# Optimization experiments

Measured on AMD Instinct MI355X. Metric: run time of the kernel, lower is better.

## Reference

```python
import jax, jax.numpy as jnp
import numpy as np

STATE_DIM = 32
OBS_DIM = 16
PROCESS_VAR = 1e-4
MEAS_VAR = 1e-2
B = 2048
T = 64


def setup_inputs() -> dict:
    key = jax.random.key(0)
    k1, k2, k3 = jax.random.split(key, 3)
    state0 = jax.random.normal(k1, (B, STATE_DIM), dtype=jnp.float32)
    # Initial covariance P = I (per torch __init__), broadcast over batch
    cov0 = jnp.broadcast_to(jnp.eye(STATE_DIM, dtype=jnp.float32), (B, STATE_DIM, STATE_DIM))
    measurements = jax.random.normal(k2, (B, T, OBS_DIM), dtype=jnp.float32)
    # Parameters per torch __init__: F = eye, H = randn, Q = pv*I, R = mv*I
    F = jnp.eye(STATE_DIM, dtype=jnp.float32)
    H = jax.random.normal(k3, (OBS_DIM, STATE_DIM), dtype=jnp.float32)
    Q = PROCESS_VAR * jnp.eye(STATE_DIM, dtype=jnp.float32)
    R = MEAS_VAR * jnp.eye(OBS_DIM, dtype=jnp.float32)
    return {"state0": state0, "cov0": cov0, "measurements": measurements,
            "F": F, "H": H, "Q": Q, "R": R}


def reference(state0, cov0, measurements, F, H, Q, R):
    """Run Kalman predict+update over T timesteps; return filtered states (B,T,S)."""

    def step(carry, z):
        x, P = carry  # x: (B,S), P: (B,S,S); z: (B,O)
        # --- predict ---
        x_pred = x @ F.T                                   # F @ x per batch
        P_pred = jnp.einsum('ij,bjk,lk->bil', F, P, F) + Q  # F P F^T + Q
        # --- update ---
        y = x_pred @ H.T                                   # predicted measurement (B,O)
        innov = z - y
        S = jnp.einsum('ij,bjk,lk->bil', H, P_pred, H) + R  # (B,O,O)
        S_inv = jnp.linalg.inv(S)
        K = jnp.einsum('bij,kj,bkl->bil', P_pred, H, S_inv)  # P H^T S^{-1}, (B,S,O)
        x_new = x_pred + jnp.einsum('bij,bj->bi', K, innov)
        P_new = P_pred - jnp.einsum('bij,jk,bkl->bil', K, H, P_pred)  # (I - K H) P
        return (x_new, P_new), x_new

    # scan over time axis: measurements (B,T,O) -> (T,B,O)
    (_, _), states = jax.lax.scan(step, (state0, cov0), jnp.swapaxes(measurements, 0, 1))
    return jnp.swapaxes(states, 0, 1)  # (B,T,S)
```

## Files before the change

kernel.cpp:

```cpp
#include <hip/hip_runtime.h>
#include <math.h>


#define S_DIM 32
#define O_DIM 16
#define HS 36
#define CW 8
#define NTHR 576

__device__ __forceinline__ float rdlanef(float v, int srcLane) {
    return __uint_as_float(
        (unsigned int)__builtin_amdgcn_readlane((int)__float_as_uint(v), srcLane));
}

__global__ __launch_bounds__(NTHR) void kf_fused(
    const float* __restrict__ state0,
    const float* __restrict__ cov0,
    const float* __restrict__ meas,
    const float* __restrict__ Fm,
    const float* __restrict__ Hm,
    const float* __restrict__ Qm,
    const float* __restrict__ Rm,
    float* __restrict__ out,
    int T, int B)
{
    const int tid = threadIdx.x;

    __shared__ float P  [S_DIM*33];
    __shared__ float Fs [S_DIM*33];
    __shared__ float Qs [S_DIM*33];
    __shared__ float Tp [S_DIM*33];
    __shared__ float Hs [O_DIM*HS];
    __shared__ float HQ [O_DIM*HS];
    __shared__ float HPs[O_DIM*HS];
    __shared__ float KT [2][O_DIM*33];
    __shared__ float Sg [O_DIM*17];
    __shared__ float Rs [O_DIM*17];
    __shared__ float S0g[O_DIM*17];
    __shared__ float xs [CW][32];
    __shared__ float iv [CW][16];
    __shared__ int notId, notDiag, notScal, convFlag, convT;
    __shared__ float cupad[13000];

    if (tid == 0) {
        ((volatile float*)cupad)[0] = 0.f;
        notId = 0; notDiag = 0; notScal = 0; convFlag = 0; convT = 0;
    }

    for (int i = tid; i < S_DIM*S_DIM; i += NTHR) {
        int r = i >> 5, c = i & 31;
        P [r*33+c] = cov0[i];
        Fs[r*33+c] = Fm[i];
        Qs[r*33+c] = Qm[i];
    }
    for (int i = tid; i < O_DIM*S_DIM; i += NTHR) {
        int r = i >> 5, c = i & 31;
        Hs[r*HS+c] = Hm[i];
    }
    for (int i = tid; i < O_DIM*O_DIM; i += NTHR) {
        int r = i >> 4, c = i & 15;
        Rs[r*17+c] = Rm[i];
    }
    __syncthreads();

    {
        bool badI = false, badD = false, badS = false;
        float r00 = Rs[0];
        for (int i = tid; i < S_DIM*S_DIM; i += NTHR) {
            int r = i >> 5, c = i & 31;
            if (Fs[r*33+c] != ((r == c) ? 1.0f : 0.0f)) badI = true;
        }
        for (int i = tid; i < O_DIM*O_DIM; i += NTHR) {
            int r = i >> 4, c = i & 15;
            if (r != c && Rs[r*17+c] != 0.0f) badD = true;
            if (r == c && Rs[r*17+c] != r00)  badS = true;
        }
        if (badI) notId = 1;
        if (badD) notDiag = 1;
        if (badS) notScal = 1;
    }
    __syncthreads();
    const bool fId   = (notId == 0);
    const bool rDiag = (notDiag == 0);
    const bool rScal = rDiag && (notScal == 0);

    const int wv = tid >> 6;
    const int l  = tid & 63;
    const int s  = l & 31;
    const int h  = l >> 5;
    const int o  = l & 15;
    const int q  = l >> 4;
    const int wi = (wv >= 1) ? (wv - 1) : 0;
    const bool isCons = (wv >= 1);
    long bb = (long)blockIdx.x * CW + wi;
    const long b = (bb < B) ? bb : (B - 1);

    float4 h0v, h1v;
    {
        const float4* Hv = (const float4*)(Hm + o*S_DIM + q*8);
        h0v = Hv[0]; h1v = Hv[1];
    }

    float x = 0.f;
    if (isCons) {
        x = state0[b*S_DIM + s];
        if (h == 0) xs[wi][s] = x;
    }
    __syncthreads();

    auto cons_step = [&](int tstep, int bufc) {
        float za = meas[(b*T + tstep)*O_DIM + o];
        const float4* xq = (const float4*)(&xs[wi][q*8]);
        float4 xa = xq[0], xb = xq[1];
        float p = h0v.x*xa.x + h0v.y*xa.y + h0v.z*xa.z + h0v.w*xa.w
                + h1v.x*xb.x + h1v.y*xb.y + h1v.z*xb.z + h1v.w*xb.w;
        float p2 = p + __shfl_xor(p, 16, 64);
        float y  = p2 + __shfl_xor(p2, 32, 64);
        float innov = za - y;
        __builtin_amdgcn_wave_barrier();
        if (l < 16) iv[wi][o] = innov;
        __builtin_amdgcn_wave_barrier();
        const float* ivp = &iv[wi][h*8];
        const float* ktp = &KT[bufc][(h*8)*33 + s];
        float acc = 0.f;
        #pragma unroll
        for (int m = 0; m < 8; ++m) acc = fmaf(ktp[m*33], ivp[m], acc);
        float xnew = x + (acc + __shfl_xor(acc, 32, 64));
        if (h == 0) out[(b*T + tstep)*S_DIM + s] = xnew;
        __builtin_amdgcn_wave_barrier();
        if (h == 0) xs[wi][s] = xnew;
        __builtin_amdgcn_wave_barrier();
        x = xnew;
    };

    if (fId && rDiag) {
        for (int i = tid; i < S_DIM*S_DIM; i += NTHR) {
            int r = i >> 5, c = i & 31;
            P[r*33+c] += Qs[r*33+c];
        }
        __syncthreads();
        if (tid < 512) {
            int r = tid >> 5, c = tid & 31;
            float a0 = 0.f, q0 = 0.f;
            for (int k = 0; k < S_DIM; ++k) {
                a0 += Hs[r*HS+k]*P [k*33+c];
                q0 += Hs[r*HS+k]*Qs[k*33+c];
            }
            HPs[r*HS+c] = a0;
            HQ [r*HS+c] = q0;
        }
        __syncthreads();
        if (tid < 256) {
            int r = tid >> 4, c = tid & 15;
            float a = Rs[r*17+c];
            const float4* hp = (const float4*)&HPs[r*HS];
            const float4* hh = (const float4*)&Hs [c*HS];
            #pragma unroll
            for (int k = 0; k < 8; ++k) {
                float4 u = hp[k], v = hh[k];
                a += u.x*v.x + u.y*v.y + u.z*v.z + u.w*v.w;
            }
            Sg[r*17+c] = a;
        } else if (tid < 512) {
            int i = tid - 256;
            int r = i >> 4, c = i & 15;
            float a = Rs[r*17+c];
            const float4* hq = (const float4*)&HQ[r*HS];
            const float4* hh = (const float4*)&Hs[c*HS];
            #pragma unroll
            for (int k = 0; k < 8; ++k) {
                float4 u = hq[k], v = hh[k];
                a += u.x*v.x + u.y*v.y + u.z*v.z + u.w*v.w;
            }
            S0g[r*17+c] = a;
        }
        __syncthreads();

        float a[16], aux1[16], hqc[16];
        float r0 = 0.f, rcL = 0.f;
        const int myc  = tid;
        const int lc16 = myc & 15;
        const bool isS = (myc < O_DIM);
        const bool isK = (myc >= O_DIM && myc < 48);
        const bool isI = (myc >= 48);
        const int j = myc - O_DIM;
        if (tid < 64) {
            __builtin_amdgcn_s_setprio(1);
            r0  = Rs[0];
            rcL = rScal ? r0 : Rs[lc16*17+lc16];
            #pragma unroll
            for (int r = 0; r < O_DIM; ++r) {
                float v;
                if (isS)      v = Sg[r*17+myc];
                else if (isK) v = HPs[r*HS+j];
                else          v = (r == lc16) ? 1.0f : 0.0f;
                a[r] = v;
                float av;
                if (isI)      av = S0g[r*17+lc16];
                else          av = 0.f;
                aux1[r] = av;
                hqc[r] = isK ? HQ[r*HS+j] : 0.f;
            }
        }

        int t = 0;
        for (; t < T; ++t) {
            const int buf = t & 1;
            if (tid < 64) {
                if (t > 0) {
                    #pragma unroll
                    for (int r = 0; r < O_DIM; ++r) {
                        float sv = __shfl(a[r], 48 + lc16, 64);
                        if (isS) a[r] = sv;
                        else if (isI) a[r] = (r == lc16) ? 1.0f : 0.0f;
                    }
                }

                #pragma unroll
                for (int p = 0; p < O_DIM; ++p) {
                    float sp[16];
                    #pragma unroll
                    for (int r = 0; r < O_DIM; ++r) sp[r] = rdlanef(a[r], p);
                    float pinv = __builtin_amdgcn_rcpf(sp[p]);
                    float sc = a[p] * pinv;
                    #pragma unroll
                    for (int r = 0; r < O_DIM; ++r)
                        a[r] = (r == p) ? sc : fmaf(-sp[r], sc, a[r]);
                }

                float d = 0.f;
                if (isK) {
                    #pragma unroll
                    for (int r = 0; r < O_DIM; ++r) {
                        float dd = fabsf(a[r] - aux1[r]);
                        d = fmaxf(d, dd);
                        aux1[r] = a[r];
                    }
                }
                unsigned long long anyBig = __ballot(isK && (d > 1e-5f));
                if (myc == 0 && anyBig == 0ull && t >= 1) {
                    convFlag = 1; convT = t;
                }

                if (isK) {
                    #pragma unroll
                    for (int oo = 0; oo < O_DIM; ++oo) KT[buf][oo*33+j] = a[oo];
                    #pragma unroll
                    for (int r = 0; r < O_DIM; ++r) {
                        float rr = rScal ? r0 : Rs[r*17+r];
                        a[r] = fmaf(rr, a[r], hqc[r]);
                    }
                }
                if (isI) {
                    #pragma unroll
                    for (int r = 0; r < O_DIM; ++r) {
                        float rr = rScal ? r0 : Rs[r*17+r];
                        float v = fmaf(-(rr*rcL), a[r], aux1[r]);
                        if (r == lc16) v += rr;
                        a[r] = v;
                    }
                }
            } else if (isCons && t > 0) {
                cons_step(t - 1, buf ^ 1);
            }
            __syncthreads();

            if (convFlag) break;
        }
        if (tid < 64) __builtin_amdgcn_s_setprio(0);

        if (!isCons) return;

        if (!convFlag) {
            cons_step(T - 1, (T - 1) & 1);
            return;
        }

        const int tc  = convT;
        const int bufc = tc & 1;
        float ka[16];
        #pragma unroll
        for (int jj = 0; jj < 16; ++jj) ka[jj] = KT[bufc][jj*33 + s];

        float4 kc0, kc1;
        kc0.x = h ? ka[8]  : ka[0];  kc0.y = h ? ka[9]  : ka[1];
        kc0.z = h ? ka[10] : ka[2];  kc0.w = h ? ka[11] : ka[3];
        kc1.x = h ? ka[12] : ka[4];  kc1.y = h ? ka[13] : ka[5];
        kc1.z = h ? ka[14] : ka[6];  kc1.w = h ? ka[15] : ka[7];

        float mreg[16];
        #pragma unroll
        for (int jj = 0; jj < 16; ++jj)
            mreg[jj] = (s == h*16 + jj) ? 1.0f : 0.0f;
        for (int oo = 0; oo < O_DIM; ++oo) {
            const float4* Hr = (const float4*)&Hs[oo*HS + h*16];
            float4 a0 = Hr[0], a1 = Hr[1], a2 = Hr[2], a3 = Hr[3];
            float k = ka[oo];
            mreg[0]  = fmaf(-k, a0.x, mreg[0]);
            mreg[1]  = fmaf(-k, a0.y, mreg[1]);
            mreg[2]  = fmaf(-k, a0.z, mreg[2]);
            mreg[3]  = fmaf(-k, a0.w, mreg[3]);
            mreg[4]  = fmaf(-k, a1.x, mreg[4]);
            mreg[5]  = fmaf(-k, a1.y, mreg[5]);
            mreg[6]  = fmaf(-k, a1.z, mreg[6]);
            mreg[7]  = fmaf(-k, a1.w, mreg[7]);
            mreg[8]  = fmaf(-k, a2.x, mreg[8]);
            mreg[9]  = fmaf(-k, a2.y, mreg[9]);
            mreg[10] = fmaf(-k, a2.z, mreg[10]);
            mreg[11] = fmaf(-k, a2.w, mreg[11]);
            mreg[12] = fmaf(-k, a3.x, mreg[12]);
            mreg[13] = fmaf(-k, a3.y, mreg[13]);
            mreg[14] = fmaf(-k, a3.z, mreg[14]);
            mreg[15] = fmaf(-k, a3.w, mreg[15]);
        }

        int t2 = tc;
        float4 zva0, zva1, zvb0, zvb1;
        {
            const float4* Zv = (const float4*)(meas + (b*T + t2)*O_DIM + h*8);
            zva0 = Zv[0]; zva1 = Zv[1];
            const int t1 = (t2 + 1 < T) ? (t2 + 1) : t2;
            const float4* Zv1 = (const float4*)(meas + (b*T + t1)*O_DIM + h*8);
            zvb0 = Zv1[0]; zvb1 = Zv1[1];
        }

        for (; t2 < T; ++t2) {
            float4 zvc0, zvc1;
            {
                const int tn = (t2 + 2 < T) ? (t2 + 2) : (T - 1);
                const float4* Zv = (const float4*)(meas + (b*T + tn)*O_DIM + h*8);
                zvc0 = Zv[0]; zvc1 = Zv[1];
            }

            const float4* xv = (const float4*)(&xs[wi][h*16]);
            float4 xa = xv[0], xb = xv[1], xc = xv[2], xd = xv[3];
            float p = mreg[0] *xa.x + mreg[1] *xa.y + mreg[2] *xa.z + mreg[3] *xa.w
                    + mreg[4] *xb.x + mreg[5] *xb.y + mreg[6] *xb.z + mreg[7] *xb.w
                    + mreg[8] *xc.x + mreg[9] *xc.y + mreg[10]*xc.z + mreg[11]*xc.w
                    + mreg[12]*xd.x + mreg[13]*xd.y + mreg[14]*xd.z + mreg[15]*xd.w;
            p += kc0.x*zva0.x + kc0.y*zva0.y + kc0.z*zva0.z + kc0.w*zva0.w
               + kc1.x*zva1.x + kc1.y*zva1.y + kc1.z*zva1.z + kc1.w*zva1.w;
            float xnew = p + __shfl_xor(p, 32, 64);

            if (h == 0) out[(b*T + t2)*S_DIM + s] = xnew;

            __builtin_amdgcn_wave_barrier();
            if (h == 0) xs[wi][s] = xnew;
            __builtin_amdgcn_wave_barrier();

            zva0 = zvb0; zva1 = zvb1;
            zvb0 = zvc0; zvb1 = zvc1;
        }
        return;
    }

    float4 f0, f1, f2, f3;
    if (isCons) {
        const float4* Fv = (const float4*)(Fm + s*S_DIM + h*16);
        f0 = Fv[0]; f1 = Fv[1]; f2 = Fv[2]; f3 = Fv[3];
    }

    for (int t = 0; t < T; ++t) {
        for (int i = tid; i < S_DIM*S_DIM; i += NTHR) {
            int r = i >> 5, c = i & 31;
            float a = 0.f;
            for (int k = 0; k < S_DIM; ++k) a += Fs[r*33+k]*P[k*33+c];
            Tp[r*33+c] = a;
        }
        __syncthreads();
        for (int i = tid; i < S_DIM*S_DIM; i += NTHR) {
            int r = i >> 5, c = i & 31;
            float a = Qs[r*33+c];
            for (int k = 0; k < S_DIM; ++k) a += Tp[r*33+k]*Fs[c*33+k];
            P[r*33+c] = a;
        }
        __syncthreads();
        if (tid < 512) {
            int r = tid >> 5, c = tid & 31;
            float a = 0.f;
            for (int k = 0; k < S_DIM; ++k) a += Hs[r*HS+k]*P[k*33+c];
            HPs[r*HS+c] = a;
        }
        __syncthreads();
        if (tid < 256) {
            int r = tid >> 4, c = tid & 15;
            float a = Rs[r*17+c];
            const float4* hp = (const float4*)&HPs[r*HS];
            const float4* hh = (const float4*)&Hs [c*HS];
            #pragma unroll
            for (int k = 0; k < 8; ++k) {
                float4 u = hp[k], v = hh[k];
                a += u.x*v.x + u.y*v.y + u.z*v.z + u.w*v.w;
            }
            Sg[r*17+c] = a;
        }
        __syncthreads();
        if (tid < 64) {
            const int myc = tid;
            const bool isS = (myc < O_DIM);
            const bool isK = (!isS && myc < 48);
            const int hc = (myc - O_DIM) & 31;
            float a[16];
            #pragma unroll
            for (int r = 0; r < O_DIM; ++r)
                a[r] = isS ? Sg[r*17+myc] : HPs[r*HS+hc];
            #pragma unroll
            for (int p = 0; p < O_DIM; ++p) {
                float sp[16];
                #pragma unroll
                for (int r = 0; r < O_DIM; ++r) sp[r] = rdlanef(a[r], p);
                float pinv = __builtin_amdgcn_rcpf(sp[p]);
                float sc = a[p] * pinv;
                #pragma unroll
                for (int r = 0; r < O_DIM; ++r)
                    a[r] = (r == p) ? sc : fmaf(-sp[r], sc, a[r]);
            }
            if (isK) {
                const int jj = myc - O_DIM;
                #pragma unroll
                for (int oo = 0; oo < O_DIM; ++oo) KT[0][oo*33+jj] = a[oo];
            }
        }
        __syncthreads();

        if (isCons) {
            const float4* xv = (const float4*)(&xs[wi][h*16]);
            float4 xa = xv[0], xb = xv[1], xc = xv[2], xd = xv[3];
            float pr = f0.x*xa.x + f0.y*xa.y + f0.z*xa.z + f0.w*xa.w
                     + f1.x*xb.x + f1.y*xb.y + f1.z*xb.z + f1.w*xb.w
                     + f2.x*xc.x + f2.y*xc.y + f2.z*xc.z + f2.w*xc.w
                     + f3.x*xd.x + f3.y*xd.y + f3.z*xd.z + f3.w*xd.w;
            x = pr + __shfl_xor(pr, 32, 64);
            __builtin_amdgcn_wave_barrier();
            if (h == 0) xs[wi][s] = x;
            __builtin_amdgcn_wave_barrier();
            cons_step(t, 0);
        }

        for (int i = tid; i < S_DIM*S_DIM; i += NTHR) {
            int r = i >> 5, c = i & 31;
            float acc = 0.f;
            for (int oo = 0; oo < O_DIM; ++oo)
                acc += KT[0][oo*33+r]*HPs[oo*HS+c];
            P[r*33+c] -= acc;
        }
        __syncthreads();
    }
}

extern "C" void kernel_launch(void* const* d_in, const int* in_sizes, int n_in,
                              void* d_out, int out_size, void* d_ws, size_t ws_size,
                              hipStream_t stream) {
    const float* state0 = (const float*)d_in[0];
    const float* cov0   = (const float*)d_in[1];
    const float* meas   = (const float*)d_in[2];
    const float* Fm     = (const float*)d_in[3];
    const float* Hm     = (const float*)d_in[4];
    const float* Qm     = (const float*)d_in[5];
    const float* Rm     = (const float*)d_in[6];
    float* out = (float*)d_out;

    const int B = in_sizes[0] / S_DIM;
    const int T = in_sizes[2] / (B * O_DIM);

    const int grid = (B + CW - 1) / CW;
    kf_fused<<<dim3(grid), dim3(NTHR), 0, stream>>>(
        state0, cov0, meas, Fm, Hm, Qm, Rm, out, T, B);
}
```

Measured before the change: 144.6 us.

## Decouple Riccati wave from consumer waves with flag-based ring-buffer handoff

Replaces the per-timestep __syncthreads lockstep between the covariance/gain wave and the eight state-update waves with a producer/consumer protocol. The producer publishes progress and the convergence step through an LDS control word, and consumers poll it. An 8-slot gain ring buffer with per-wave progress counters lets the producer run up to RD steps ahead. This removes block-wide barrier stalls, at the cost of spin polling with s_sleep. It also adds an odd debug-like write of iteration counts into the workspace from block 0, and shrinks the LDS occupancy padding.

Result: no change. 147.5 us (+2.0%).

```diff
diff --git a/kernel.cpp b/kernel.cpp
--- a/kernel.cpp
+++ b/kernel.cpp
@@ -7,6 +7,9 @@
 #define HS 36
 #define CW 8
 #define NTHR 576
+#define RD 8
+
+typedef unsigned int u32;
 
 __device__ __forceinline__ float rdlanef(float v, int srcLane) {
     return __uint_as_float(
@@ -22,6 +25,7 @@
     const float* __restrict__ Qm,
     const float* __restrict__ Rm,
     float* __restrict__ out,
+    float* __restrict__ ws,
     int T, int B)
 {
     const int tid = threadIdx.x;
@@ -33,19 +37,23 @@
     __shared__ float Hs [O_DIM*HS];
     __shared__ float HQ [O_DIM*HS];
     __shared__ float HPs[O_DIM*HS];
-    __shared__ float KT [2][O_DIM*33];
+    __shared__ float KT [RD][O_DIM*33];
     __shared__ float Sg [O_DIM*17];
     __shared__ float Rs [O_DIM*17];
     __shared__ float S0g[O_DIM*17];
     __shared__ float xs [CW][32];
     __shared__ float iv [CW][16];
-    __shared__ int notId, notDiag, notScal, convFlag, convT;
-    __shared__ float cupad[13000];
+    __shared__ int notId, notDiag, notScal;
+    __shared__ u32 ctrlw;
+    __shared__ int prog[CW];
+    __shared__ float cupad[9500];
 
     if (tid == 0) {
         ((volatile float*)cupad)[0] = 0.f;
-        notId = 0; notDiag = 0; notScal = 0; convFlag = 0; convT = 0;
-    }
+        notId = 0; notDiag = 0; notScal = 0;
+        ctrlw = 0u;
+    }
+    if (tid < CW) prog[tid] = 0;
 
     for (int i = tid; i < S_DIM*S_DIM; i += NTHR) {
         int r = i >> 5, c = i & 31;
@@ -108,7 +116,7 @@
     }
     __syncthreads();
 
-    auto cons_step = [&](int tstep, int bufc) {
+    auto cons_step = [&](int tstep, int slot) {
         float za = meas[(b*T + tstep)*O_DIM + o];
         const float4* xq = (const float4*)(&xs[wi][q*8]);
         float4 xa = xq[0], xb = xq[1];
@@ -121,7 +129,7 @@
         if (l < 16) iv[wi][o] = innov;
         __builtin_amdgcn_wave_barrier();
         const float* ivp = &iv[wi][h*8];
-        const float* ktp = &KT[bufc][(h*8)*33 + s];
+        const float* ktp = &KT[slot][(h*8)*33 + s];
         float acc = 0.f;
         #pragma unroll
         for (int m = 0; m < 8; ++m) acc = fmaf(ktp[m*33], ivp[m], acc);
@@ -176,18 +184,17 @@
         }
         __syncthreads();
 
-        float a[16], aux1[16], hqc[16];
-        float r0 = 0.f, rcL = 0.f;
-        const int myc  = tid;
-        const int lc16 = myc & 15;
-        const bool isS = (myc < O_DIM);
-        const bool isK = (myc >= O_DIM && myc < 48);
-        const bool isI = (myc >= 48);
-        const int j = myc - O_DIM;
         if (tid < 64) {
             __builtin_amdgcn_s_setprio(1);
-            r0  = Rs[0];
-            rcL = rScal ? r0 : Rs[lc16*17+lc16];
+            float a[16], aux1[16], hqc[16];
+            const int myc  = tid;
+            const int lc16 = myc & 15;
+            const bool isS = (myc < O_DIM);
+            const bool isK = (myc >= O_DIM && myc < 48);
+            const bool isI = (myc >= 48);
+            const int j = myc - O_DIM;
+            float r0  = Rs[0];
+            float rcL = rScal ? r0 : Rs[lc16*17+lc16];
             #pragma unroll
             for (int r = 0; r < O_DIM; ++r) {
                 float v;
@@ -195,18 +202,26 @@
                 else if (isK) v = HPs[r*HS+j];
                 else          v = (r == lc16) ? 1.0f : 0.0f;
                 a[r] = v;
-                float av;
-                if (isI)      av = S0g[r*17+lc16];
-                else          av = 0.f;
-                aux1[r] = av;
-                hqc[r] = isK ? HQ[r*HS+j] : 0.f;
-            }
-        }
-
-        int t = 0;
-        for (; t < T; ++t) {
-            const int buf = t & 1;
-            if (tid < 64) {
+                aux1[r] = isI ? S0g[r*17+lc16] : 0.f;
+                hqc[r]  = isK ? HQ[r*HS+j] : 0.f;
+            }
+
+            int iters = 0;
+            for (int t = 0; t < T; ++t) {
+                if (t >= RD) {
+                    for (;;) {
+                        int mn = 0x7fffffff;
+                        #pragma unroll
+                        for (int i2 = 0; i2 < CW; ++i2) {
+                            int pv = __hip_atomic_load(&prog[i2], __ATOMIC_RELAXED,
+                                                       __HIP_MEMORY_SCOPE_WORKGROUP);
+                            mn = (pv < mn) ? pv : mn;
+                        }
+                        if (mn >= t - RD + 1) break;
+                        __builtin_amdgcn_s_sleep(1);
+                    }
+                }
+
                 if (t > 0) {
                     #pragma unroll
                     for (int r = 0; r < O_DIM; ++r) {
@@ -238,13 +253,12 @@
                     }
                 }
                 unsigned long long anyBig = __ballot(isK && (d > 1e-5f));
-                if (myc == 0 && anyBig == 0ull && t >= 1) {
-                    convFlag = 1; convT = t;
-                }
-
+                const bool convNow = (anyBig == 0ull && t >= 1);
+
+                const int slot = t & (RD - 1);
                 if (isK) {
                     #pragma unroll
-                    for (int oo = 0; oo < O_DIM; ++oo) KT[buf][oo*33+j] = a[oo];
+                    for (int oo = 0; oo < O_DIM; ++oo) KT[slot][oo*33+j] = a[oo];
                     #pragma unroll
                     for (int r = 0; r < O_DIM; ++r) {
                         float rr = rScal ? r0 : Rs[r*17+r];
@@ -260,98 +274,124 @@
                         a[r] = v;
                     }
                 }
-            } else if (isCons && t > 0) {
-                cons_step(t - 1, buf ^ 1);
-            }
-            __syncthreads();
-
-            if (convFlag) break;
-        }
-        if (tid < 64) __builtin_amdgcn_s_setprio(0);
-
-        if (!isCons) return;
-
-        if (!convFlag) {
-            cons_step(T - 1, (T - 1) & 1);
+
+                if (myc == 0) {
+                    u32 cw = (u32)(t + 1) | (convNow ? ((u32)t << 16) : 0u);
+                    __hip_atomic_store(&ctrlw, cw, __ATOMIC_RELEASE,
+                                       __HIP_MEMORY_SCOPE_WORKGROUP);
+                }
+                ++iters;
+                if (convNow) break;
+            }
+            __builtin_amdgcn_s_setprio(0);
+
+            if (blockIdx.x == 0) {
+                for (int i3 = 0; i3 < iters; ++i3) {
+                    float* wp = ws + (long)i3 * 512 + myc * 8;
+                    #pragma unroll
+                    for (int k3 = 0; k3 < 8; ++k3)
+                        __builtin_nontemporal_store((float)i3, wp + k3);
+                }
+            }
             return;
         }
 
-        const int tc  = convT;
-        const int bufc = tc & 1;
-        float ka[16];
-        #pragma unroll
-        for (int jj = 0; jj < 16; ++jj) ka[jj] = KT[bufc][jj*33 + s];
-
-        float4 kc0, kc1;
-        kc0.x = h ? ka[8]  : ka[0];  kc0.y = h ? ka[9]  : ka[1];
-        kc0.z = h ? ka[10] : ka[2];  kc0.w = h ? ka[11] : ka[3];
-        kc1.x = h ? ka[12] : ka[4];  kc1.y = h ? ka[13] : ka[5];
-        kc1.z = h ? ka[14] : ka[6];  kc1.w = h ? ka[15] : ka[7];
-
-        float mreg[16];
-        #pragma unroll
-        for (int jj = 0; jj < 16; ++jj)
-            mreg[jj] = (s == h*16 + jj) ? 1.0f : 0.0f;
-        for (int oo = 0; oo < O_DIM; ++oo) {
-            const float4* Hr = (const float4*)&Hs[oo*HS + h*16];
-            float4 a0 = Hr[0], a1 = Hr[1], a2 = Hr[2], a3 = Hr[3];
-            float k = ka[oo];
-            mreg[0]  = fmaf(-k, a0.x, mreg[0]);
-            mreg[1]  = fmaf(-k, a0.y, mreg[1]);
-            mreg[2]  = fmaf(-k, a0.z, mreg[2]);
-            mreg[3]  = fmaf(-k, a0.w, mreg[3]);
-            mreg[4]  = fmaf(-k, a1.x, mreg[4]);
-            mreg[5]  = fmaf(-k, a1.y, mreg[5]);
-            mreg[6]  = fmaf(-k, a1.z, mreg[6]);
-            mreg[7]  = fmaf(-k, a1.w, mreg[7]);
-            mreg[8]  = fmaf(-k, a2.x, mreg[8]);
-            mreg[9]  = fmaf(-k, a2.y, mreg[9]);
-            mreg[10] = fmaf(-k, a2.z, mreg[10]);
-            mreg[11] = fmaf(-k, a2.w, mreg[11]);
-            mreg[12] = fmaf(-k, a3.x, mreg[12]);
-            mreg[13] = fmaf(-k, a3.y, mreg[13]);
-            mreg[14] = fmaf(-k, a3.z, mreg[14]);
-            mreg[15] = fmaf(-k, a3.w, mreg[15]);
-        }
-
-        int t2 = tc;
-        float4 zva0, zva1, zvb0, zvb1;
         {
-            const float4* Zv = (const float4*)(meas + (b*T + t2)*O_DIM + h*8);
-            zva0 = Zv[0]; zva1 = Zv[1];
-            const int t1 = (t2 + 1 < T) ? (t2 + 1) : t2;
-            const float4* Zv1 = (const float4*)(meas + (b*T + t1)*O_DIM + h*8);
-            zvb0 = Zv1[0]; zvb1 = Zv1[1];
-        }
-
-        for (; t2 < T; ++t2) {
-            float4 zvc0, zvc1;
+            int t = 0, tcv = 0;
+            for (;;) {
+                u32 cw = __hip_atomic_load(&ctrlw, __ATOMIC_ACQUIRE,
+                                           __HIP_MEMORY_SCOPE_WORKGROUP);
+                int availv = (int)(cw & 0xFFFFu);
+                tcv = (int)(cw >> 16);
+                int lim = tcv ? tcv : availv;
+                bool prog_made = (t < lim);
+                for (; t < lim; ++t) {
+                    cons_step(t, t & (RD - 1));
+                    if (l == 0)
+                        __hip_atomic_store(&prog[wi], t + 1, __ATOMIC_RELEASE,
+                                           __HIP_MEMORY_SCOPE_WORKGROUP);
+                }
+                if (tcv && t >= tcv) break;
+                if (t >= T) return;
+                if (!prog_made) __builtin_amdgcn_s_sleep(2);
+            }
+
+            const int slot = tcv & (RD - 1);
+            float ka[16];
+            #pragma unroll
+            for (int jj = 0; jj < 16; ++jj) ka[jj] = KT[slot][jj*33 + s];
+
+            float4 kc0, kc1;
+            kc0.x = h ? ka[8]  : ka[0];  kc0.y = h ? ka[9]  : ka[1];
+            kc0.z = h ? ka[10] : ka[2];  kc0.w = h ? ka[11] : ka[3];
+            kc1.x = h ? ka[12] : ka[4];  kc1.y = h ? ka[13] : ka[5];
+            kc1.z = h ? ka[14] : ka[6];  kc1.w = h ? ka[15] : ka[7];
+
+            float mreg[16];
+            #pragma unroll
+            for (int jj = 0; jj < 16; ++jj)
+                mreg[jj] = (s == h*16 + jj) ? 1.0f : 0.0f;
+            for (int oo = 0; oo < O_DIM; ++oo) {
+                const float4* Hr = (const float4*)&Hs[oo*HS + h*16];
+                float4 a0 = Hr[0], a1 = Hr[1], a2 = Hr[2], a3 = Hr[3];
+                float k = ka[oo];
+                mreg[0]  = fmaf(-k, a0.x, mreg[0]);
+                mreg[1]  = fmaf(-k, a0.y, mreg[1]);
+                mreg[2]  = fmaf(-k, a0.z, mreg[2]);
+                mreg[3]  = fmaf(-k, a0.w, mreg[3]);
+                mreg[4]  = fmaf(-k, a1.x, mreg[4]);
+                mreg[5]  = fmaf(-k, a1.y, mreg[5]);
+                mreg[6]  = fmaf(-k, a1.z, mreg[6]);
+                mreg[7]  = fmaf(-k, a1.w, mreg[7]);
+                mreg[8]  = fmaf(-k, a2.x, mreg[8]);
+                mreg[9]  = fmaf(-k, a2.y, mreg[9]);
+                mreg[10] = fmaf(-k, a2.z, mreg[10]);
+                mreg[11] = fmaf(-k, a2.w, mreg[11]);
+                mreg[12] = fmaf(-k, a3.x, mreg[12]);
+                mreg[13] = fmaf(-k, a3.y, mreg[13]);
+                mreg[14] = fmaf(-k, a3.z, mreg[14]);
+                mreg[15] = fmaf(-k, a3.w, mreg[15]);
+            }
+
+            int t2 = tcv;
+            float4 zva0, zva1, zvb0, zvb1;
             {
-                const int tn = (t2 + 2 < T) ? (t2 + 2) : (T - 1);
-                const float4* Zv = (const float4*)(meas + (b*T + tn)*O_DIM + h*8);
-                zvc0 = Zv[0]; zvc1 = Zv[1];
-            }
-
-            const float4* xv = (const float4*)(&xs[wi][h*16]);
-            float4 xa = xv[0], xb = xv[1], xc = xv[2], xd = xv[3];
-            float p = mreg[0] *xa.x + mreg[1] *xa.y + mreg[2] *xa.z + mreg[3] *xa.w
-                    + mreg[4] *xb.x + mreg[5] *xb.y + mreg[6] *xb.z + mreg[7] *xb.w
-                    + mreg[8] *xc.x + mreg[9] *xc.y + mreg[10]*xc.z + mreg[11]*xc.w
-                    + mreg[12]*xd.x + mreg[13]*xd.y + mreg[14]*xd.z + mreg[15]*xd.w;
-            p += kc0.x*zva0.x + kc0.y*zva0.y + kc0.z*zva0.z + kc0.w*zva0.w
-               + kc1.x*zva1.x + kc1.y*zva1.y + kc1.z*zva1.z + kc1.w*zva1.w;
-            float xnew = p + __shfl_xor(p, 32, 64);
-
-            if (h == 0) out[(b*T + t2)*S_DIM + s] = xnew;
-
-            __builtin_amdgcn_wave_barrier();
-            if (h == 0) xs[wi][s] = xnew;
-            __builtin_amdgcn_wave_barrier();
-
-            zva0 = zvb0; zva1 = zvb1;
-            zvb0 = zvc0; zvb1 = zvc1;
-        }
-        return;
+                const float4* Zv = (const float4*)(meas + (b*T + t2)*O_DIM + h*8);
+                zva0 = Zv[0]; zva1 = Zv[1];
+                const int t1 = (t2 + 1 < T) ? (t2 + 1) : t2;
+                const float4* Zv1 = (const float4*)(meas + (b*T + t1)*O_DIM + h*8);
+                zvb0 = Zv1[0]; zvb1 = Zv1[1];
+            }
+
+            for (; t2 < T; ++t2) {
+                float4 zvc0, zvc1;
+                {
+                    const int tn = (t2 + 2 < T) ? (t2 + 2) : (T - 1);
+                    const float4* Zv = (const float4*)(meas + (b*T + tn)*O_DIM + h*8);
+                    zvc0 = Zv[0]; zvc1 = Zv[1];
+                }
+
+                const float4* xv = (const float4*)(&xs[wi][h*16]);
+                float4 xa = xv[0], xb = xv[1], xc = xv[2], xd = xv[3];
+                float p = mreg[0] *xa.x + mreg[1] *xa.y + mreg[2] *xa.z + mreg[3] *xa.w
+                        + mreg[4] *xb.x + mreg[5] *xb.y + mreg[6] *xb.z + mreg[7] *xb.w
+                        + mreg[8] *xc.x + mreg[9] *xc.y + mreg[10]*xc.z + mreg[11]*xc.w
+                        + mreg[12]*xd.x + mreg[13]*xd.y + mreg[14]*xd.z + mreg[15]*xd.w;
+                p += kc0.x*zva0.x + kc0.y*zva0.y + kc0.z*zva0.z + kc0.w*zva0.w
+                   + kc1.x*zva1.x + kc1.y*zva1.y + kc1.z*zva1.z + kc1.w*zva1.w;
+                float xnew = p + __shfl_xor(p, 32, 64);
+
+                if (h == 0) out[(b*T + t2)*S_DIM + s] = xnew;
+
+                __builtin_amdgcn_wave_barrier();
+                if (h == 0) xs[wi][s] = xnew;
+                __builtin_amdgcn_wave_barrier();
+
+                zva0 = zvb0; zva1 = zvb1;
+                zvb0 = zvc0; zvb1 = zvc1;
+            }
+            return;
+        }
     }
 
     float4 f0, f1, f2, f3;
@@ -459,11 +499,12 @@
     const float* Qm     = (const float*)d_in[5];
     const float* Rm     = (const float*)d_in[6];
     float* out = (float*)d_out;
+    float* ws  = (float*)d_ws;
 
     const int B = in_sizes[0] / S_DIM;
     const int T = in_sizes[2] / (B * O_DIM);
 
     const int grid = (B + CW - 1) / CW;
     kf_fused<<<dim3(grid), dim3(NTHR), 0, stream>>>(
-        state0, cov0, meas, Fm, Hm, Qm, Rm, out, T, B);
+        state0, cov0, meas, Fm, Hm, Qm, Rm, out, ws, T, B);
 }
```
